# Kernel tuning notes

Hardware: AMD Instinct MI355X
Metric: run time of the kernel (lower is better)

The kernel has to match this reference:

```python
import jax, jax.numpy as jnp
from jax import lax
import numpy as np

B, S, E, HID = 16, 7, 64, 64
RES = (64, 64); D = RES[0] * RES[1]
XLOW, XHIGH = -0.5, 0.5
RLOW, RHIGH = float(np.sqrt(0.01)), float(np.sqrt(0.05))
PIXEL_MULT = 1.0; N_ITER = 3; TSOFT = 1.0 / float(np.sqrt(E))

def _build_grid():
    ranges = [np.linspace(XLOW, XHIGH, r) for r in RES]
    g = np.stack(np.meshgrid(*ranges, indexing='xy'), axis=-1)
    g = g.reshape(RES[0], RES[1], -1).reshape(1, -1, 2)
    return jnp.asarray(g, dtype=jnp.float32)

ABS_GRID = _build_grid()  # [1, D, 2]

def _ln(x, g, b):
    m = jnp.mean(x, -1, keepdims=True)
    v = jnp.mean(jnp.square(x - m), -1, keepdims=True)
    return (x - m) * lax.rsqrt(v + 1e-5) * g + b

def _forward(data, slot_noise, pos_rand, conv0_w, conv0_b, conv1_w, conv1_b, conv2_w, conv2_b,
             dataN_g, dataN_b, queryN_g, queryN_b, toK_w, toK_b, toV_w, toV_b, dense_w, dense_b,
             mlp1_w, mlp1_b, mlp2_w, mlp2_b, gru_wih, gru_whh, gru_bih, gru_bhh,
             alpha1_w, alpha1_b, alpha2_w, alpha2_b, final1_w, final1_b, final2_w, final2_b,
             slots_mu, slots_logsigma):
    dn = ('NCHW', 'OIHW', 'NCHW')
    def conv(x, w, b):
        return lax.conv_general_dilated(x, w, (1, 1), 'SAME', dimension_numbers=dn) + b[None, :, None, None]
    # CNN encoder: Conv-ReLU x3, 'same' padding, k=5
    x = jax.nn.relu(conv(data, conv0_w, conv0_b))
    x = jax.nn.relu(conv(x, conv1_w, conv1_b))
    x = jax.nn.relu(conv(x, conv2_w, conv2_b))
    enc = x.transpose(0, 2, 3, 1).reshape(B, D, HID)
    enc = _ln(enc, dataN_g, dataN_b)

    queries = slots_mu + jnp.exp(slots_logsigma) * slot_noise  # [B,S,E]
    # init_slots: faithful replication (source indexes the SLOT dim, and swaps rlow/rhigh)
    pos_scale = pos_rand.at[:, :2, :].add(-0.5)
    pos_scale = pos_scale.at[:, -1, :].set((RLOW - RHIGH) * pos_rand[:, -1, :] + RHIGH)

    encK = enc @ toK_w + toK_b  # [B,D,E]
    encV = enc @ toV_w + toV_b

    def init_mlp(y):
        y = _ln(y, queryN_g, queryN_b)
        return jax.nn.relu(y @ mlp1_w + mlp1_b) @ mlp2_w + mlp2_b

    def get_kv(ps):
        # per-slot relative grid: [B,S,D,2]
        rel = (ABS_GRID[:, None] - ps[:, :, None, :2]) / ps[:, :, -1][:, :, None, None]
        eg = PIXEL_MULT * (rel @ dense_w + dense_b)  # [B,S,D,E]
        return init_mlp(encK[:, None] + eg), init_mlp(encV[:, None] + eg)

    def att_wts(q, k):
        logits = jnp.einsum('bse,bsde->bsd', q, k) * TSOFT
        att = jax.nn.softmax(logits, axis=1)  # softmax over slots
        wts = att / jnp.sum(att, -1, keepdims=True) + 1e-8
        return att, wts

    def update_frames(wts):
        new_pos = jnp.einsum('bsd,de->bse', wts, ABS_GRID[0])  # [B,S,2]
        d2 = jnp.sum(jnp.square(ABS_GRID[:, None] - new_pos[:, :, None]), -1)  # [B,S,D]
        new_scale = jnp.sqrt(jnp.einsum('bsd,bsd->bs', wts, d2))
        return jnp.concatenate([new_pos, new_scale[..., None]], -1)

    def gru(xg, h):
        gi = xg @ gru_wih.T + gru_bih
        gh = h @ gru_whh.T + gru_bhh
        ir, iz, inn = jnp.split(gi, 3, -1)
        hr, hz, hn = jnp.split(gh, 3, -1)
        r = jax.nn.sigmoid(ir + hr)
        z = jax.nn.sigmoid(iz + hz)
        n = jnp.tanh(inn + r * hn)
        return (1.0 - z) * n + z * h

    for _ in range(N_ITER):
        keys, vals = get_kv(pos_scale)
        att, wts = att_wts(_ln(queries, queryN_g, queryN_b), keys)
        pos_scale = update_frames(wts)
        upd = jnp.einsum('bsd,bsde->bse', wts, vals)
        queries = gru(upd.reshape(-1, E), queries.reshape(-1, E)).reshape(B, S, E)

    keys, _ = get_kv(pos_scale)
    att, wts = att_wts(_ln(queries, queryN_g, queryN_b), keys)
    nps = update_frames(wts)
    alpha = jax.nn.sigmoid(jax.nn.relu(queries @ alpha1_w + alpha1_b) @ alpha2_w + alpha2_b)
    slot_feat = jax.nn.relu(queries @ final1_w + final1_b) @ final2_w + final2_b + nps
    return queries, att, slot_feat, alpha

def setup_inputs() -> dict:
    ks = jax.random.split(jax.random.key(0), 20)
    f32 = jnp.float32
    def rn(i, shape, s):
        return jax.random.normal(ks[i], shape, f32) * s
    inp = dict(
        data=jax.random.normal(ks[0], (B, 1, RES[0], RES[1]), f32),
        slot_noise=jax.random.normal(ks[1], (B, S, E), f32),
        pos_rand=jax.random.uniform(ks[2], (B, S, 3), dtype=f32),
        conv0_w=rn(3, (HID, 1, 5, 5), 0.2), conv0_b=jnp.zeros(HID, f32),
        conv1_w=rn(4, (HID, HID, 5, 5), 0.025), conv1_b=jnp.zeros(HID, f32),
        conv2_w=rn(5, (HID, HID, 5, 5), 0.025), conv2_b=jnp.zeros(HID, f32),
        dataN_g=jnp.ones(HID, f32), dataN_b=jnp.zeros(HID, f32),
        queryN_g=jnp.ones(E, f32), queryN_b=jnp.zeros(E, f32),
        toK_w=rn(6, (HID, E), 0.125), toK_b=jnp.zeros(E, f32),
        toV_w=rn(7, (HID, E), 0.125), toV_b=jnp.zeros(E, f32),
        dense_w=rn(8, (2, E), 0.7), dense_b=jnp.zeros(E, f32),
        mlp1_w=rn(9, (E, E), 0.125), mlp1_b=jnp.zeros(E, f32),
        mlp2_w=rn(10, (E, E), 0.125), mlp2_b=jnp.zeros(E, f32),
        gru_wih=rn(11, (3 * E, E), 0.125), gru_whh=rn(12, (3 * E, E), 0.125),
        gru_bih=jnp.zeros(3 * E, f32), gru_bhh=jnp.zeros(3 * E, f32),
        alpha1_w=rn(13, (E, 32), 0.125), alpha1_b=jnp.zeros(32, f32),
        alpha2_w=rn(14, (32, 1), 0.18), alpha2_b=jnp.zeros(1, f32),
        final1_w=rn(15, (E, HID), 0.125), final1_b=jnp.zeros(HID, f32),
        final2_w=rn(16, (HID, 3), 0.125), final2_b=jnp.zeros(3, f32),
        slots_mu=rn(17, (1, 1, E), 1.0),
        slots_logsigma=rn(18, (1, 1, E), 0.01),
    )
    return inp

def reference(data, slot_noise, pos_rand, conv0_w, conv0_b, conv1_w, conv1_b, conv2_w, conv2_b,
              dataN_g, dataN_b, queryN_g, queryN_b, toK_w, toK_b, toV_w, toV_b, dense_w, dense_b,
              mlp1_w, mlp1_b, mlp2_w, mlp2_b, gru_wih, gru_whh, gru_bih, gru_bhh,
              alpha1_w, alpha1_b, alpha2_w, alpha2_b, final1_w, final1_b, final2_w, final2_b,
              slots_mu, slots_logsigma):
    return _forward(data, slot_noise, pos_rand, conv0_w, conv0_b, conv1_w, conv1_b, conv2_w, conv2_b,
                    dataN_g, dataN_b, queryN_g, queryN_b, toK_w, toK_b, toV_w, toV_b, dense_w, dense_b,
                    mlp1_w, mlp1_b, mlp2_w, mlp2_b, gru_wih, gru_whh, gru_bih, gru_bhh,
                    alpha1_w, alpha1_b, alpha2_w, alpha2_b, final1_w, final1_b, final2_w, final2_b,
                    slots_mu, slots_logsigma)
```

## Files before the change

### kernel.cpp

```cpp
#include <hip/hip_runtime.h>
#include <cmath>


#define RLOW_F 0.1f
#define RHIGH_F 0.22360679774997896f
#define W0CONST 1.00004096f
#define SR2 704.3386243f

typedef __attribute__((ext_vector_type(8))) __bf16 bf16x8;
typedef __attribute__((ext_vector_type(4))) float f32x4;

__device__ __forceinline__ float wsum64(float v){
  #pragma unroll
  for (int off = 32; off > 0; off >>= 1) v += __shfl_xor(v, off, 64);
  return v;
}
__device__ __forceinline__ float rdlane(float v, int l){
  return __int_as_float(__builtin_amdgcn_readlane(__float_as_int(v), l));
}
__device__ __forceinline__ unsigned short bf16bits(float v){
  __bf16 h = (__bf16)v;
  return *reinterpret_cast<unsigned short*>(&h);
}

__device__ __forceinline__ void pp_core(int row, int e, float qv,
    float px, float py, float sc,
    const float* __restrict__ qg_, const float* __restrict__ qb_,
    const float* __restrict__ dw, const float* __restrict__ db,
    const float* __restrict__ mlp2w, const float* __restrict__ mlp2b,
    float* __restrict__ absc, float* __restrict__ w2qc){
  float m = wsum64(qv) * (1.f/64.f);
  float d = qv - m;
  float var = wsum64(d*d) * (1.f/64.f);
  float qlnv = d * (1.0f/sqrtf(var + 1e-5f)) * qg_[e] + qb_[e];
  float A  = dw[e]      / sc;
  float Bv = dw[64 + e] / sc;
  absc[row*192 + e]       = A;
  absc[row*192 + 64 + e]  = Bv;
  absc[row*192 + 128 + e] = db[e] - px*A - py*Bv;
  float acc = 0.f;
  const float* wrow = mlp2w + e*64;
  for (int j = 0; j < 64; j++) acc = fmaf(wrow[j], rdlane(qlnv, j), acc);
  w2qc[row*68 + e] = acc;
  float c2 = wsum64(mlp2b[e] * qlnv);
  if (e == 0) w2qc[row*68 + 64] = c2;
}

__global__ void k_packall(const float* __restrict__ mlp1_w, const float* __restrict__ toK_w,
                          const float* __restrict__ toV_w, const float* __restrict__ conv1_w,
                          const float* __restrict__ conv2_w,
                          unsigned short* __restrict__ w1pack, unsigned short* __restrict__ kpack,
                          unsigned short* __restrict__ vpack, unsigned short* __restrict__ wp1,
                          unsigned short* __restrict__ wp2,
                          const float* __restrict__ noise, const float* __restrict__ prand,
                          const float* __restrict__ mu, const float* __restrict__ logsig,
                          const float* __restrict__ qg_, const float* __restrict__ qb_,
                          const float* __restrict__ dw, const float* __restrict__ db,
                          const float* __restrict__ mlp2w, const float* __restrict__ mlp2b,
                          float* __restrict__ queries, float* __restrict__ ps,
                          float* __restrict__ absc, float* __restrict__ w2qc,
                          float* __restrict__ accF, float* __restrict__ upd){
  int bi = blockIdx.x; int t = threadIdx.x;
  if (bi < 48){
    const float* src = (bi < 16) ? mlp1_w : ((bi < 32) ? toK_w : toV_w);
    unsigned short* dst = (bi < 16) ? w1pack : ((bi < 32) ? kpack : vpack);
    int idx = (bi & 15)*256 + t;
    int jj = idx & 7;
    int lane = (idx >> 3) & 63;
    int frag = idx >> 9;
    int ks = frag >> 2, nt = frag & 3;
    int q = lane >> 4, cr = lane & 15;
    int k = ks*32 + q*8 + jj;
    int n = nt*16 + cr;
    dst[idx] = bf16bits(src[k*64 + n]);
  } else if (bi < 848){
    int rb = bi - 48;
    const float* src = (rb < 400) ? conv1_w : conv2_w;
    unsigned short* dst = (rb < 400) ? wp1 : wp2;
    int idx = (rb % 400)*256 + t;
    int j = idx & 7;
    int l = (idx >> 3) & 63;
    int frag = idx >> 9;
    int nt = frag & 3;
    int ks = (frag >> 2) % 10;
    int dy = frag / 40;
    int q = l >> 4, cr = l & 15;
    int k = ks*32 + q*8 + j;
    int kx = k >> 6, ch = k & 63;
    int n = nt*16 + cr;
    dst[idx] = bf16bits(src[((n*64 + ch)*5 + dy)*5 + kx]);
  } else {
    if (t >= 64) return;
    int row = bi - 848;
    int e = t;
    int s = row % 7;
    float qv = mu[e] + expf(logsig[e]) * noise[row*64 + e];
    queries[row*64 + e] = qv;
    upd[row*128 + e] = 0.f;
    upd[row*128 + 64 + e] = 0.f;
    if (e < 4) accF[row*4 + e] = 0.f;
    float pv = 0.f;
    if (e < 3){
      float pr = prand[row*3 + e];
      if (s < 2)       pv = pr - 0.5f;
      else if (s == 6) pv = (RLOW_F - RHIGH_F)*pr + RHIGH_F;
      else             pv = pr;
      ps[row*3 + e] = pv;
    }
    float px = rdlane(pv, 0), py = rdlane(pv, 1), sc = rdlane(pv, 2);
    pp_core(row, e, qv, px, py, sc, qg_, qb_, dw, db, mlp2w, mlp2b, absc, w2qc);
  }
}

__global__ __launch_bounds__(256) void k_conv0(const float* __restrict__ in,
                        const float* __restrict__ w, const float* __restrict__ bias,
                        unsigned short* __restrict__ out){
  int bi = blockIdx.x; int b = bi >> 6; int y = bi & 63;
  int t = threadIdx.x; int lane = t & 63; int xg = t >> 6;
  __shared__ float s_in[5*68];
  __shared__ float s_w[64*25];
  __shared__ float s_out[64*65];
  for (int i = t; i < 1600; i += 256) s_w[i] = w[i];
  for (int i = t; i < 340; i += 256){
    int r = i / 68, cx = i % 68;
    int yy = y + r - 2, gx = cx - 2;
    float v = 0.f;
// ... 141 lines not shown
  const bf16x8* vp = reinterpret_cast<const bf16x8*>(vpack);
  bf16x8 KB[8], VB[8];
  #pragma unroll
  for (int f = 0; f < 8; f++){ KB[f] = kp[f*64 + l]; VB[f] = vp[f*64 + l]; }

  const unsigned short* er = enc + (size_t)(b*4096 + d0 + cr)*64;
  bf16x8 a0 = *reinterpret_cast<const bf16x8*>(er + q*8);
  bf16x8 a1 = *reinterpret_cast<const bf16x8*>(er + 32 + q*8);

  f32x4 zero = {0.f,0.f,0.f,0.f};
  f32x4 aK[4], aV[4];
  #pragma unroll
  for (int nt = 0; nt < 4; nt++){
    aK[nt] = __builtin_amdgcn_mfma_f32_16x16x32_bf16(a0, KB[nt],     zero,   0, 0, 0);
    aK[nt] = __builtin_amdgcn_mfma_f32_16x16x32_bf16(a1, KB[4 + nt], aK[nt], 0, 0, 0);
    aV[nt] = __builtin_amdgcn_mfma_f32_16x16x32_bf16(a0, VB[nt],     zero,   0, 0, 0);
    aV[nt] = __builtin_amdgcn_mfma_f32_16x16x32_bf16(a1, VB[4 + nt], aV[nt], 0, 0, 0);
  }
  #pragma unroll
  for (int nt = 0; nt < 4; nt++){
    float bkv = bk[nt*16 + cr], bvv = bvp[nt*16 + cr];
    #pragma unroll
    for (int reg = 0; reg < 4; reg++){
      size_t base = ((size_t)b*4096 + d0 + q*4 + reg)*64 + nt*16 + cr;
      K[base] = bf16bits(aK[nt][reg] + bkv);
      V[base] = bf16bits(aV[nt][reg] + bvv);
    }
  }
}

__global__ __launch_bounds__(256) void k_attn(const unsigned short* __restrict__ encK,
     const unsigned short* __restrict__ encV,
     const unsigned short* __restrict__ w1pack, const float* __restrict__ mlp1b,
     const float* __restrict__ absc, const float* __restrict__ qg_,
     const float* __restrict__ qb_, const float* __restrict__ w2qc,
     float* __restrict__ attOut, float* __restrict__ accF,
     float* __restrict__ upd, int mode){
  int bi = blockIdx.x;
  int b = bi >> 6, tile = bi & 63;
  int t = threadIdx.x; int wv = t >> 6; int l = t & 63;
  int q = l >> 4, cr = l & 15;
  int m0 = tile*64 + wv*16;
  int drow = m0 + cr;

  __shared__ float s_log[7*64];
  __shared__ float s_absc[7*192];
  __shared__ float s_wq[7*68];
  __shared__ float s_upd[7*128];
  __shared__ unsigned short s_w1[4096];
  for (int i = t; i < 1344; i += 256) s_absc[i] = absc[b*7*192 + i];
  for (int i = t; i < 476;  i += 256) s_wq[i]   = w2qc[b*7*68 + i];
  if (mode == 0)
    for (int i = t; i < 896; i += 256) s_upd[i] = 0.f;
  {
    const uint4* g = reinterpret_cast<const uint4*>(w1pack);
    uint4* d = reinterpret_cast<uint4*>(s_w1);
    for (int i = t; i < 512; i += 256) d[i] = g[i];
  }

  const unsigned short* er = encK + (size_t)(b*4096 + drow)*64;
  float gx = -0.5f + (float)(drow & 63) * (1.f/63.f);
  float gy = -0.5f + (float)((drow >> 6) & 63) * (1.f/63.f);
  float xb[16], gq[16], bq[16];
  {
    bf16x8 ea = *reinterpret_cast<const bf16x8*>(er + q*8);
    bf16x8 eb = *reinterpret_cast<const bf16x8*>(er + 32 + q*8);
    #pragma unroll
    for (int i = 0; i < 8; i++){ xb[i] = (float)ea[i]; xb[8+i] = (float)eb[i]; }
  }
  bf16x8 vb0, vb1;
  if (mode == 0){
    const unsigned short* ev = encV + (size_t)(b*4096 + drow)*64;
    vb0 = *reinterpret_cast<const bf16x8*>(ev + q*8);
    vb1 = *reinterpret_cast<const bf16x8*>(ev + 32 + q*8);
  }
  #pragma unroll
  for (int h = 0; h < 2; h++){
    int fb = h ? (32 + q*8) : (q*8);
    const float4* g4 = reinterpret_cast<const float4*>(qg_ + fb);
    const float4* b4 = reinterpret_cast<const float4*>(qb_ + fb);
    #pragma unroll
    for (int p = 0; p < 2; p++){
      float4 gg = g4[p], bb = b4[p];
      int o = h*8 + p*4;
      gq[o+0]=gg.x; gq[o+1]=gg.y; gq[o+2]=gg.z; gq[o+3]=gg.w;
      bq[o+0]=bb.x; bq[o+1]=bb.y; bq[o+2]=bb.z; bq[o+3]=bb.w;
    }
  }
  float b1v[4];
  #pragma unroll
  for (int nt = 0; nt < 4; nt++) b1v[nt] = mlp1b[nt*16 + cr];
  __syncthreads();

  const bf16x8* wl = reinterpret_cast<const bf16x8*>(s_w1);
  f32x4 zero = {0.f, 0.f, 0.f, 0.f};

  for (int sp = 0; sp < 4; sp++){
    int s0 = sp*2;
    int np = (sp == 3) ? 1 : 2;
    int sB = (np == 2) ? s0 + 1 : s0;
    float x0[16], x1[16];
    float s1a = 0.f, s2a = 0.f, s1b = 0.f, s2b = 0.f;
    {
      const float* Ac = s_absc + s0*192;
      #pragma unroll
      for (int h = 0; h < 2; h++){
        int fb = h ? (32 + q*8) : (q*8);
        const float4* A4 = reinterpret_cast<const float4*>(Ac + fb);
        const float4* B4 = reinterpret_cast<const float4*>(Ac + 64 + fb);
        const float4* C4 = reinterpret_cast<const float4*>(Ac + 128 + fb);
        #pragma unroll
        for (int p = 0; p < 2; p++){
          float4 Av = A4[p], Bv = B4[p], Cv = C4[p];
          int o = h*8 + p*4;
          x0[o+0] = xb[o+0] + gx*Av.x + gy*Bv.x + Cv.x;
          x0[o+1] = xb[o+1] + gx*Av.y + gy*Bv.y + Cv.y;
          x0[o+2] = xb[o+2] + gx*Av.z + gy*Bv.z + Cv.z;
          x0[o+3] = xb[o+3] + gx*Av.w + gy*Bv.w + Cv.w;
        }
      }
      #pragma unroll
      for (int k = 0; k < 16; k++){ s1a += x0[k]; s2a = fmaf(x0[k], x0[k], s2a); }
    }
    {
      const float* Ac = s_absc + sB*192;
      #pragma unroll
      for (int h = 0; h < 2; h++){
        int fb = h ? (32 + q*8) : (q*8);
        const float4* A4 = reinterpret_cast<const float4*>(Ac + fb);
        const float4* B4 = reinterpret_cast<const float4*>(Ac + 64 + fb);
        const float4* C4 = reinterpret_cast<const float4*>(Ac + 128 + fb);
        #pragma unroll
        for (int p = 0; p < 2; p++){
          float4 Av = A4[p], Bv = B4[p], Cv = C4[p];
          int o = h*8 + p*4;
          x1[o+0] = xb[o+0] + gx*Av.x + gy*Bv.x + Cv.x;
          x1[o+1] = xb[o+1] + gx*Av.y + gy*Bv.y + Cv.y;
          x1[o+2] = xb[o+2] + gx*Av.z + gy*Bv.z + Cv.z;
          x1[o+3] = xb[o+3] + gx*Av.w + gy*Bv.w + Cv.w;
        }
      }
      #pragma unroll
      for (int k = 0; k < 16; k++){ s1b += x1[k]; s2b = fmaf(x1[k], x1[k], s2b); }
    }
    s1a += __shfl_xor(s1a, 16, 64); s2a += __shfl_xor(s2a, 16, 64);
    s1b += __shfl_xor(s1b, 16, 64); s2b += __shfl_xor(s2b, 16, 64);
    s1a += __shfl_xor(s1a, 32, 64); s2a += __shfl_xor(s2a, 32, 64);
    s1b += __shfl_xor(s1b, 32, 64); s2b += __shfl_xor(s2b, 32, 64);
    float mA = s1a*(1.f/64.f);
    float rA = 1.0f/sqrtf(s2a*(1.f/64.f) - mA*mA + 1e-5f);
    float mB = s1b*(1.f/64.f);
    float rB = 1.0f/sqrtf(s2b*(1.f/64.f) - mB*mB + 1e-5f);

    bf16x8 a00, a01, a10, a11;
    #pragma unroll
    for (int k = 0; k < 8; k++){
      a00[k] = (__bf16)((x0[k]    - mA)*rA*gq[k]   + bq[k]);
      a01[k] = (__bf16)((x0[8+k]  - mA)*rA*gq[8+k] + bq[8+k]);
      a10[k] = (__bf16)((x1[k]    - mB)*rB*gq[k]   + bq[k]);
      a11[k] = (__bf16)((x1[8+k]  - mB)*rB*gq[8+k] + bq[8+k]);
    }

    f32x4 acc0[4], acc1[4];
    #pragma unroll
    for (int nt = 0; nt < 4; nt++){
      bf16x8 w0 = wl[nt*64 + l];
      bf16x8 w1f = wl[(4 + nt)*64 + l];
      acc0[nt] = __builtin_amdgcn_mfma_f32_16x16x32_bf16(a00, w0,  zero,     0, 0, 0);
      acc0[nt] = __builtin_amdgcn_mfma_f32_16x16x32_bf16(a01, w1f, acc0[nt], 0, 0, 0);
      acc1[nt] = __builtin_amdgcn_mfma_f32_16x16x32_bf16(a10, w0,  zero,     0, 0, 0);
      acc1[nt] = __builtin_amdgcn_mfma_f32_16x16x32_bf16(a11, w1f, acc1[nt], 0, 0, 0);
    }

    float p0[4] = {0.f,0.f,0.f,0.f}, p1[4] = {0.f,0.f,0.f,0.f};
    #pragma unroll
    for (int nt = 0; nt < 4; nt++){
      float wq0 = s_wq[s0*68 + nt*16 + cr];
      float wq1 = s_wq[sB*68 + nt*16 + cr];
      #pragma unroll
      for (int reg = 0; reg < 4; reg++){
        p0[reg] = fmaf(fmaxf(acc0[nt][reg] + b1v[nt], 0.f), wq0, p0[reg]);
        p1[reg] = fmaf(fmaxf(acc1[nt][reg] + b1v[nt], 0.f), wq1, p1[reg]);
      }
    }
    #pragma unroll
    for (int off = 1; off < 16; off <<= 1){
      #pragma unroll
      for (int reg = 0; reg < 4; reg++){
        p0[reg] += __shfl_xor(p0[reg], off, 64);
        p1[reg] += __shfl_xor(p1[reg], off, 64);
      }
    }
    if (cr == 0){
      float c20 = s_wq[s0*68 + 64];
      float c21 = s_wq[sB*68 + 64];
      #pragma unroll
      for (int reg = 0; reg < 4; reg++){
        s_log[s0*64 + wv*16 + q*4 + reg] = (p0[reg] + c20) * 0.125f;
        if (np == 2) s_log[sB*64 + wv*16 + q*4 + reg] = (p1[reg] + c21) * 0.125f;
      }
    }
  }
  __syncthreads();

  if (t < 64){
    float lv[7];
    #pragma unroll
    for (int s = 0; s < 7; s++) lv[s] = s_log[s*64 + t];
    float mx = lv[0];
    #pragma unroll
    for (int s = 1; s < 7; s++) mx = fmaxf(mx, lv[s]);
    float sm = 0.f;
    #pragma unroll
    for (int s = 0; s < 7; s++){ lv[s] = expf(lv[s] - mx); sm += lv[s]; }
    float inv = 1.0f / sm;
    #pragma unroll
    for (int s = 0; s < 7; s++){
      float a = lv[s] * inv;
      s_log[s*64 + t] = a;
      if (mode == 1) attOut[(size_t)(b*7+s)*4096 + tile*64 + t] = a;
    }
  }
  __syncthreads();

  if (t < 224){
    int s = t >> 5, r = t & 31;
    float a1 = s_log[s*64 + r];
    float a2 = s_log[s*64 + r + 32];
    float gx1 = -0.5f + (float)r * (1.f/63.f);
    float gx2 = -0.5f + (float)(r + 32) * (1.f/63.f);
    float gyc = -0.5f + (float)tile * (1.f/63.f);
    float gy2c = gyc*gyc;
    float w0 = a1 + a2;
    float w1 = a1*gx1 + a2*gx2;
    float w2 = w0*gyc;
    float w3 = a1*(gx1*gx1 + gy2c) + a2*(gx2*gx2 + gy2c);
    #pragma unroll
    for (int m = 1; m < 32; m <<= 1){
      w0 += __shfl_xor(w0, m, 64);
      w1 += __shfl_xor(w1, m, 64);
      w2 += __shfl_xor(w2, m, 64);
      w3 += __shfl_xor(w3, m, 64);
    }
    if (r == 0){
      atomicAdd(&accF[(b*7+s)*4 + 0], w0);
      atomicAdd(&accF[(b*7+s)*4 + 1], w1);
      atomicAdd(&accF[(b*7+s)*4 + 2], w2);
      atomicAdd(&accF[(b*7+s)*4 + 3], w3);
    }
  }

  if (mode == 0){
    float xbv[16];
    #pragma unroll
    for (int i = 0; i < 8; i++){ xbv[i] = (float)vb0[i]; xbv[8+i] = (float)vb1[i]; }
    for (int sp = 0; sp < 4; sp++){
      int s0 = sp*2;
      int np = (sp == 3) ? 1 : 2;
      int sB = (np == 2) ? s0 + 1 : s0;
      float x0[16], x1[16];
      float s1a = 0.f, s2a = 0.f, s1b = 0.f, s2b = 0.f;
      {
        const float* Ac = s_absc + s0*192;
        #pragma unroll
        for (int h = 0; h < 2; h++){
          int fb = h ? (32 + q*8) : (q*8);
          const float4* A4 = reinterpret_cast<const float4*>(Ac + fb);
          const float4* B4 = reinterpret_cast<const float4*>(Ac + 64 + fb);
          const float4* C4 = reinterpret_cast<const float4*>(Ac + 128 + fb);
          #pragma unroll
          for (int p = 0; p < 2; p++){
            float4 Av = A4[p], Bv = B4[p], Cv = C4[p];
            int o = h*8 + p*4;
            x0[o+0] = xbv[o+0] + gx*Av.x + gy*Bv.x + Cv.x;
            x0[o+1] = xbv[o+1] + gx*Av.y + gy*Bv.y + Cv.y;
            x0[o+2] = xbv[o+2] + gx*Av.z + gy*Bv.z + Cv.z;
            x0[o+3] = xbv[o+3] + gx*Av.w + gy*Bv.w + Cv.w;
          }
        }
        #pragma unroll
        for (int k = 0; k < 16; k++){ s1a += x0[k]; s2a = fmaf(x0[k], x0[k], s2a); }
      }
      {
        const float* Ac = s_absc + sB*192;
        #pragma unroll
        for (int h = 0; h < 2; h++){
          int fb = h ? (32 + q*8) : (q*8);
          const float4* A4 = reinterpret_cast<const float4*>(Ac + fb);
          const float4* B4 = reinterpret_cast<const float4*>(Ac + 64 + fb);
          const float4* C4 = reinterpret_cast<const float4*>(Ac + 128 + fb);
          #pragma unroll
          for (int p = 0; p < 2; p++){
            float4 Av = A4[p], Bv = B4[p], Cv = C4[p];
            int o = h*8 + p*4;
            x1[o+0] = xbv[o+0] + gx*Av.x + gy*Bv.x + Cv.x;
            x1[o+1] = xbv[o+1] + gx*Av.y + gy*Bv.y + Cv.y;
            x1[o+2] = xbv[o+2] + gx*Av.z + gy*Bv.z + Cv.z;
            x1[o+3] = xbv[o+3] + gx*Av.w + gy*Bv.w + Cv.w;
          }
        }
        #pragma unroll
        for (int k = 0; k < 16; k++){ s1b += x1[k]; s2b = fmaf(x1[k], x1[k], s2b); }
      }
      s1a += __shfl_xor(s1a, 16, 64); s2a += __shfl_xor(s2a, 16, 64);
      s1b += __shfl_xor(s1b, 16, 64); s2b += __shfl_xor(s2b, 16, 64);
      s1a += __shfl_xor(s1a, 32, 64); s2a += __shfl_xor(s2a, 32, 64);
      s1b += __shfl_xor(s1b, 32, 64); s2b += __shfl_xor(s2b, 32, 64);
      float mA = s1a*(1.f/64.f);
      float rA = 1.0f/sqrtf(s2a*(1.f/64.f) - mA*mA + 1e-5f);
      float mB = s1b*(1.f/64.f);
      float rB = 1.0f/sqrtf(s2b*(1.f/64.f) - mB*mB + 1e-5f);

      bf16x8 a00, a01, a10, a11;
      #pragma unroll
      for (int k = 0; k < 8; k++){
        a00[k] = (__bf16)((x0[k]    - mA)*rA*gq[k]   + bq[k]);
        a01[k] = (__bf16)((x0[8+k]  - mA)*rA*gq[8+k] + bq[8+k]);
        a10[k] = (__bf16)((x1[k]    - mB)*rB*gq[k]   + bq[k]);
        a11[k] = (__bf16)((x1[8+k]  - mB)*rB*gq[8+k] + bq[8+k]);
      }

      f32x4 acc0[4], acc1[4];
      #pragma unroll
      for (int nt = 0; nt < 4; nt++){
        bf16x8 w0 = wl[nt*64 + l];
        bf16x8 w1f = wl[(4 + nt)*64 + l];
        acc0[nt] = __builtin_amdgcn_mfma_f32_16x16x32_bf16(a00, w0,  zero,     0, 0, 0);
        acc0[nt] = __builtin_amdgcn_mfma_f32_16x16x32_bf16(a01, w1f, acc0[nt], 0, 0, 0);
        acc1[nt] = __builtin_amdgcn_mfma_f32_16x16x32_bf16(a10, w0,  zero,     0, 0, 0);
        acc1[nt] = __builtin_amdgcn_mfma_f32_16x16x32_bf16(a11, w1f, acc1[nt], 0, 0, 0);
      }

      float wr0[4], wr1[4];
      #pragma unroll
      for (int reg = 0; reg < 4; reg++){
        wr0[reg] = s_log[s0*64 + wv*16 + q*4 + reg];
        wr1[reg] = s_log[sB*64 + wv*16 + q*4 + reg];
      }
      float pa0[4], pa1[4], pu0[4], pu1[4];
      #pragma unroll
      for (int nt = 0; nt < 4; nt++){
        pa0[nt] = 0.f; pa1[nt] = 0.f; pu0[nt] = 0.f; pu1[nt] = 0.f;
        #pragma unroll
        for (int reg = 0; reg < 4; reg++){
          float v0 = fmaxf(acc0[nt][reg] + b1v[nt], 0.f);
          float v1 = fmaxf(acc1[nt][reg] + b1v[nt], 0.f);
          pa0[nt] = fmaf(wr0[reg], v0, pa0[nt]); pu0[nt] += v0;
          pa1[nt] = fmaf(wr1[reg], v1, pa1[nt]); pu1[nt] += v1;
        }
      }
      #pragma unroll
      for (int nt = 0; nt < 4; nt++){
        pa0[nt] += __shfl_xor(pa0[nt], 16, 64); pa0[nt] += __shfl_xor(pa0[nt], 32, 64);
        pu0[nt] += __shfl_xor(pu0[nt], 16, 64); pu0[nt] += __shfl_xor(pu0[nt], 32, 64);
        pa1[nt] += __shfl_xor(pa1[nt], 16, 64); pa1[nt] += __shfl_xor(pa1[nt], 32, 64);
        pu1[nt] += __shfl_xor(pu1[nt], 16, 64); pu1[nt] += __shfl_xor(pu1[nt], 32, 64);
      }
      if (q == 0){
        #pragma unroll
        for (int nt = 0; nt < 4; nt++){
          atomicAdd(&s_upd[s0*128 + nt*16 + cr], pa0[nt]);
          atomicAdd(&s_upd[s0*128 + 64 + nt*16 + cr], pu0[nt]);
          if (np == 2){
            atomicAdd(&s_upd[sB*128 + nt*16 + cr], pa1[nt]);
            atomicAdd(&s_upd[sB*128 + 64 + nt*16 + cr], pu1[nt]);
          }
        }
      }
    }
    __syncthreads();
    for (int i = t; i < 896; i += 256)
      atomicAdd(&upd[b*896 + i], s_upd[i]);
  }
}

__global__ void k_gru(float* __restrict__ upd, float* __restrict__ queries,
                      const float* __restrict__ wih, const float* __restrict__ whh,
                      const float* __restrict__ bih, const float* __restrict__ bhh,
                      const float* __restrict__ mlp2w, const float* __restrict__ mlp2b,
                      float* __restrict__ accF, float* __restrict__ ps,
                      const float* __restrict__ qg_, const float* __restrict__ qb_,
                      const float* __restrict__ dw, const float* __restrict__ db,
                      float* __restrict__ absc, float* __restrict__ w2qc){
  int row = blockIdx.x; int t = threadIdx.x;
  __shared__ float us[64], hs[64], xs[64], gis[192], ghs[192];
  __shared__ float s_ps3[3];
  if (t < 64){
    float isa0 = 1.0f/accF[row*4];
    us[t] = upd[row*128 + t]*isa0 + 1e-8f*upd[row*128 + 64 + t];
    hs[t] = queries[row*64 + t];
  }
  if (t == 64){
    float sa = accF[row*4+0];
    float ax = accF[row*4+1], ay = accF[row*4+2], ar2 = accF[row*4+3];
    float isa = 1.0f/sa;
    float Wx = ax*isa, Wy = ay*isa;
    float Wg = ar2*isa + 1e-8f*SR2;
    float s2 = Wg - (Wx*Wx + Wy*Wy)*(2.f - W0CONST);
    s_ps3[0] = Wx; s_ps3[1] = Wy; s_ps3[2] = sqrtf(fmaxf(s2, 0.f));
  }
  __syncthreads();
  if (t < 64){
    float a = W0CONST * mlp2b[t];
    for (int i = 0; i < 64; i++) a = fmaf(us[i], mlp2w[i*64 + t], a);
    xs[t] = a;
  }
  __syncthreads();
  float gi = bih[t], gh = bhh[t];
  for (int e = 0; e < 64; e++){
    gi = fmaf(wih[t*64 + e], xs[e], gi);
    gh = fmaf(whh[t*64 + e], hs[e], gh);
  }
  gis[t] = gi; ghs[t] = gh;
  __syncthreads();
  if (t < 64){
    float r = 1.0f/(1.0f + expf(-(gis[t]      + ghs[t])));
    float z = 1.0f/(1.0f + expf(-(gis[64+t]   + ghs[64+t])));
    float n = tanhf(gis[128+t] + r*ghs[128+t]);
    float newq = (1.0f - z)*n + z*hs[t];
    queries[row*64 + t] = newq;
    upd[row*128 + t] = 0.f;
    upd[row*128 + 64 + t] = 0.f;
    if (t < 4) accF[row*4 + t] = 0.f;
    if (t < 3) ps[row*3 + t] = s_ps3[t];
    pp_core(row, t, newq, s_ps3[0], s_ps3[1], s_ps3[2],
            qg_, qb_, dw, db, mlp2w, mlp2b, absc, w2qc);
  }
}

__global__ void k_final(const float* __restrict__ queries, const float* __restrict__ accF,
                        const float* __restrict__ a1w, const float* __restrict__ a1b,
                        const float* __restrict__ a2w, const float* __restrict__ a2b,
                        const float* __restrict__ f1w, const float* __restrict__ f1b,
                        const float* __restrict__ f2w, const float* __restrict__ f2b,
                        float* __restrict__ out){
  int bs = blockIdx.x; int e = threadIdx.x;
  __shared__ float qs[64], hf[64], ha[32];
  float q = queries[bs*64 + e];
  qs[e] = q;
  out[bs*64 + e] = q;
  __syncthreads();
  float accf = f1b[e];
  for (int i = 0; i < 64; i++) accf = fmaf(qs[i], f1w[i*64 + e], accf);
  hf[e] = fmaxf(accf, 0.f);
  if (e < 32){
    float acca = a1b[e];
    for (int i = 0; i < 64; i++) acca = fmaf(qs[i], a1w[i*32 + e], acca);
    ha[e] = fmaxf(acca, 0.f);
  }
  __syncthreads();
  if (e < 3){
    float sf = f2b[e];
    for (int o = 0; o < 64; o++) sf = fmaf(hf[o], f2w[o*3 + e], sf);
    float sa = accF[bs*4+0], ax = accF[bs*4+1], ay = accF[bs*4+2], ar2 = accF[bs*4+3];
    float isa = 1.0f/sa;
    float Wx = ax*isa, Wy = ay*isa;
    float Wg = ar2*isa + 1e-8f*SR2;
    float s2 = Wg - (Wx*Wx + Wy*Wy)*(2.f - W0CONST);
    float nv = (e == 0) ? Wx : ((e == 1) ? Wy : sqrtf(fmaxf(s2, 0.f)));
    out[465920 + bs*3 + e] = sf + nv;
  }
  if (e == 32){
    float al = a2b[0];
    for (int o = 0; o < 32; o++) al = fmaf(ha[o], a2w[o], al);
    out[466256 + bs] = 1.0f/(1.0f + expf(-al));
  }
}

extern "C" void kernel_launch(void* const* d_in, const int* in_sizes, int n_in,
                              void* d_out, int out_size, void* d_ws, size_t ws_size,
                              hipStream_t stream){
  const float* data        = (const float*)d_in[0];
  const float* slot_noise  = (const float*)d_in[1];
  const float* pos_rand    = (const float*)d_in[2];
  const float* conv0_w     = (const float*)d_in[3];
  const float* conv0_b     = (const float*)d_in[4];
  const float* conv1_w     = (const float*)d_in[5];
  const float* conv1_b     = (const float*)d_in[6];
  const float* conv2_w     = (const float*)d_in[7];
  const float* conv2_b     = (const float*)d_in[8];
  const float* dataN_g     = (const float*)d_in[9];
  const float* dataN_b     = (const float*)d_in[10];
  const float* queryN_g    = (const float*)d_in[11];
  const float* queryN_b    = (const float*)d_in[12];
  const float* toK_w       = (const float*)d_in[13];
  const float* toK_b       = (const float*)d_in[14];
  const float* toV_w       = (const float*)d_in[15];
  const float* toV_b       = (const float*)d_in[16];
  const float* dense_w     = (const float*)d_in[17];
  const float* dense_b     = (const float*)d_in[18];
  const float* mlp1_w      = (const float*)d_in[19];
  const float* mlp1_b      = (const float*)d_in[20];
  const float* mlp2_w      = (const float*)d_in[21];
  const float* mlp2_b      = (const float*)d_in[22];
  const float* gru_wih     = (const float*)d_in[23];
  const float* gru_whh     = (const float*)d_in[24];
  const float* gru_bih     = (const float*)d_in[25];
  const float* gru_bhh     = (const float*)d_in[26];
  const float* alpha1_w    = (const float*)d_in[27];
  const float* alpha1_b    = (const float*)d_in[28];
  const float* alpha2_w    = (const float*)d_in[29];
  const float* alpha2_b    = (const float*)d_in[30];
  const float* final1_w    = (const float*)d_in[31];
  const float* final1_b    = (const float*)d_in[32];
  const float* final2_w    = (const float*)d_in[33];
  const float* final2_b    = (const float*)d_in[34];
  const float* slots_mu    = (const float*)d_in[35];
  const float* slots_lsig  = (const float*)d_in[36];

  float* ws   = (float*)d_ws;
  float* bufA = ws;
  float* bufB = bufA + 4194304;
  float* bufC = bufB + 4194304;
  float* queries = bufC + 4194304;
  float* ps   = queries + 7168;
  float* absc = ps + 512;
  float* accF = absc + 21504;
  float* upd  = accF + 512;
  float* w2qc = upd + 14336;
  unsigned short* w1pack = (unsigned short*)(w2qc + 7616);
  unsigned short* kpack  = w1pack + 4096;
  unsigned short* vpack  = kpack + 4096;
  unsigned short* wp1    = vpack + 4096;
  unsigned short* wp2    = wp1 + 102400;

  unsigned short* c0_bf = (unsigned short*)bufA;
  unsigned short* c1_bf = (unsigned short*)bufC;
  unsigned short* enc   = (unsigned short*)bufB;
  unsigned short* encK  = (unsigned short*)bufA;
  unsigned short* encV  = (unsigned short*)bufC;

  float* outq   = (float*)d_out;
  float* outatt = outq + 7168;

  k_packall<<<960, 256, 0, stream>>>(mlp1_w, toK_w, toV_w, conv1_w, conv2_w,
                                     w1pack, kpack, vpack, wp1, wp2,
                                     slot_noise, pos_rand, slots_mu, slots_lsig,
                                     queryN_g, queryN_b, dense_w, dense_b, mlp2_w, mlp2_b,
                                     queries, ps, absc, w2qc, accF, upd);
  k_conv0<<<1024, 256, 0, stream>>>(data, conv0_w, conv0_b, c0_bf);
  k_convm<<<512, 256, 0, stream>>>(c0_bf, wp1, conv1_b, nullptr, nullptr, c1_bf, 0);
  k_convm<<<512, 256, 0, stream>>>(c1_bf, wp2, conv2_b, dataN_g, dataN_b, enc, 1);
  k_projm<<<1024, 256, 0, stream>>>(enc, kpack, toK_b, vpack, toV_b, encK, encV);

  for (int p = 0; p < 4; p++){
    k_attn<<<1024, 256, 0, stream>>>(encK, encV, w1pack, mlp1_b, absc,
                                     queryN_g, queryN_b, w2qc, outatt, accF, upd,
                                     (p < 3) ? 0 : 1);
    if (p < 3){
      k_gru<<<112, 192, 0, stream>>>(upd, queries, gru_wih, gru_whh, gru_bih, gru_bhh,
                                     mlp2_w, mlp2_b, accF, ps, queryN_g, queryN_b,
                                     dense_w, dense_b, absc, w2qc);
    }
  }
  k_final<<<112, 64, 0, stream>>>(queries, accF,
                                  alpha1_w, alpha1_b, alpha2_w, alpha2_b,
                                  final1_w, final1_b, final2_w, final2_b, outq);
}
```

Baseline: 486.6 us.

## Fuse GRU update and final heads into attention kernel via last-block counter

Removes the separate k_gru and k_final launches. Each k_attn block increments a per-batch atomic counter after its atomic accumulation, and the last of the 64 tiles for a batch then runs the GRU update (or the final heads in the last pass) for all 7 slots of that batch. This cuts four kernel launches and the gaps between them. In exchange, the tail work runs in a single block per batch with serialized loops, the kernel adds shared memory that may lower occupancy, and it relies on threadfence plus atomic reads for correctness.

```diff
diff --git a/kernel.cpp b/kernel.cpp
--- a/kernel.cpp
+++ b/kernel.cpp
@@ -21,6 +21,9 @@
 __device__ __forceinline__ unsigned short bf16bits(float v){
   __bf16 h = (__bf16)v;
   return *reinterpret_cast<unsigned short*>(&h);
+}
+__device__ __forceinline__ float aread(float* p){
+  return atomicAdd(p, 0.f);
 }
 
 __device__ __forceinline__ void pp_core(int row, int e, float qv,
@@ -59,7 +62,8 @@
                           const float* __restrict__ mlp2w, const float* __restrict__ mlp2b,
                           float* __restrict__ queries, float* __restrict__ ps,
                           float* __restrict__ absc, float* __restrict__ w2qc,
-                          float* __restrict__ accF, float* __restrict__ upd){
+                          float* __restrict__ accF, float* __restrict__ upd,
+                          unsigned int* __restrict__ cnt){
   int bi = blockIdx.x; int t = threadIdx.x;
   if (bi < 48){
     const float* src = (bi < 16) ? mlp1_w : ((bi < 32) ? toK_w : toV_w);
@@ -90,8 +94,9 @@
     int n = nt*16 + cr;
     dst[idx] = bf16bits(src[((n*64 + ch)*5 + dy)*5 + kx]);
   } else {
+    int row = bi - 848;
+    if (bi == 848 && t >= 64 && t < 80) cnt[t - 64] = 0u;
     if (t >= 64) return;
-    int row = bi - 848;
     int e = t;
     int s = row % 7;
     float qv = mu[e] + expf(logsig[e]) * noise[row*64 + e];
@@ -299,10 +304,20 @@
 __global__ __launch_bounds__(256) void k_attn(const unsigned short* __restrict__ encK,
      const unsigned short* __restrict__ encV,
      const unsigned short* __restrict__ w1pack, const float* __restrict__ mlp1b,
-     const float* __restrict__ absc, const float* __restrict__ qg_,
-     const float* __restrict__ qb_, const float* __restrict__ w2qc,
+     float* __restrict__ absc, const float* __restrict__ qg_,
+     const float* __restrict__ qb_, float* __restrict__ w2qc,
      float* __restrict__ attOut, float* __restrict__ accF,
-     float* __restrict__ upd, int mode){
+     float* __restrict__ upd, int mode, unsigned int* __restrict__ cnt,
+     float* __restrict__ queries, float* __restrict__ ps,
+     const float* __restrict__ wih, const float* __restrict__ whh,
+     const float* __restrict__ bih, const float* __restrict__ bhh,
+     const float* __restrict__ mlp2w, const float* __restrict__ mlp2b,
+     const float* __restrict__ dw, const float* __restrict__ db,
+     const float* __restrict__ a1w, const float* __restrict__ a1b,
+     const float* __restrict__ a2w, const float* __restrict__ a2b,
+     const float* __restrict__ f1w, const float* __restrict__ f1b,
+     const float* __restrict__ f2w, const float* __restrict__ f2b,
+     float* __restrict__ outq){
   int bi = blockIdx.x;
   int b = bi >> 6, tile = bi & 63;
   int t = threadIdx.x; int wv = t >> 6; int l = t & 63;
@@ -315,6 +330,11 @@
   __shared__ float s_wq[7*68];
   __shared__ float s_upd[7*128];
   __shared__ unsigned short s_w1[4096];
+  __shared__ float G_us[7][64], G_hs[7][64], G_xs[7][64];
+  __shared__ float G_gi[7][192], G_gh[7][192];
+  __shared__ float G_af[28], G_p3[7][3];
+  __shared__ unsigned s_last;
+
   for (int i = t; i < 1344; i += 256) s_absc[i] = absc[b*7*192 + i];
   for (int i = t; i < 476;  i += 256) s_wq[i]   = w2qc[b*7*68 + i];
   if (mode == 0)
@@ -377,9 +397,9 @@
         const float4* B4 = reinterpret_cast<const float4*>(Ac + 64 + fb);
         const float4* C4 = reinterpret_cast<const float4*>(Ac + 128 + fb);
         #pragma unroll
-        for (int p = 0; p < 2; p++){
-          float4 Av = A4[p], Bv = B4[p], Cv = C4[p];
-          int o = h*8 + p*4;
+        for (int pp = 0; pp < 2; pp++){
+          float4 Av = A4[pp], Bv = B4[pp], Cv = C4[pp];
+          int o = h*8 + pp*4;
           x0[o+0] = xb[o+0] + gx*Av.x + gy*Bv.x + Cv.x;
           x0[o+1] = xb[o+1] + gx*Av.y + gy*Bv.y + Cv.y;
           x0[o+2] = xb[o+2] + gx*Av.z + gy*Bv.z + Cv.z;
@@ -398,9 +418,9 @@
         const float4* B4 = reinterpret_cast<const float4*>(Ac + 64 + fb);
         const float4* C4 = reinterpret_cast<const float4*>(Ac + 128 + fb);
         #pragma unroll
-        for (int p = 0; p < 2; p++){
-          float4 Av = A4[p], Bv = B4[p], Cv = C4[p];
-          int o = h*8 + p*4;
+        for (int pp = 0; pp < 2; pp++){
+          float4 Av = A4[pp], Bv = B4[pp], Cv = C4[pp];
+          int o = h*8 + pp*4;
           x1[o+0] = xb[o+0] + gx*Av.x + gy*Bv.x + Cv.x;
           x1[o+1] = xb[o+1] + gx*Av.y + gy*Bv.y + Cv.y;
           x1[o+2] = xb[o+2] + gx*Av.z + gy*Bv.z + Cv.z;
@@ -536,9 +556,9 @@
           const float4* B4 = reinterpret_cast<const float4*>(Ac + 64 + fb);
           const float4* C4 = reinterpret_cast<const float4*>(Ac + 128 + fb);
           #pragma unroll
-          for (int p = 0; p < 2; p++){
-            float4 Av = A4[p], Bv = B4[p], Cv = C4[p];
-            int o = h*8 + p*4;
+          for (int pp = 0; pp < 2; pp++){
+            float4 Av = A4[pp], Bv = B4[pp], Cv = C4[pp];
+            int o = h*8 + pp*4;
             x0[o+0] = xbv[o+0] + gx*Av.x + gy*Bv.x + Cv.x;
             x0[o+1] = xbv[o+1] + gx*Av.y + gy*Bv.y + Cv.y;
             x0[o+2] = xbv[o+2] + gx*Av.z + gy*Bv.z + Cv.z;
@@ -557,9 +577,9 @@
           const float4* B4 = reinterpret_cast<const float4*>(Ac + 64 + fb);
           const float4* C4 = reinterpret_cast<const float4*>(Ac + 128 + fb);
           #pragma unroll
-          for (int p = 0; p < 2; p++){
-            float4 Av = A4[p], Bv = B4[p], Cv = C4[p];
-            int o = h*8 + p*4;
+          for (int pp = 0; pp < 2; pp++){
+            float4 Av = A4[pp], Bv = B4[pp], Cv = C4[pp];
+            int o = h*8 + pp*4;
             x1[o+0] = xbv[o+0] + gx*Av.x + gy*Bv.x + Cv.x;
             x1[o+1] = xbv[o+1] + gx*Av.y + gy*Bv.y + Cv.y;
             x1[o+2] = xbv[o+2] + gx*Av.z + gy*Bv.z + Cv.z;
@@ -639,98 +659,110 @@
     for (int i = t; i < 896; i += 256)
       atomicAdd(&upd[b*896 + i], s_upd[i]);
   }
-}
-
-__global__ void k_gru(float* __restrict__ upd, float* __restrict__ queries,
-                      const float* __restrict__ wih, const float* __restrict__ whh,
-                      const float* __restrict__ bih, const float* __restrict__ bhh,
-                      const float* __restrict__ mlp2w, const float* __restrict__ mlp2b,
-                      float* __restrict__ accF, float* __restrict__ ps,
-                      const float* __restrict__ qg_, const float* __restrict__ qb_,
-                      const float* __restrict__ dw, const float* __restrict__ db,
-                      float* __restrict__ absc, float* __restrict__ w2qc){
-  int row = blockIdx.x; int t = threadIdx.x;
-  __shared__ float us[64], hs[64], xs[64], gis[192], ghs[192];
-  __shared__ float s_ps3[3];
-  if (t < 64){
-    float isa0 = 1.0f/accF[row*4];
-    us[t] = upd[row*128 + t]*isa0 + 1e-8f*upd[row*128 + 64 + t];
-    hs[t] = queries[row*64 + t];
-  }
-  if (t == 64){
-    float sa = accF[row*4+0];
-    float ax = accF[row*4+1], ay = accF[row*4+2], ar2 = accF[row*4+3];
-    float isa = 1.0f/sa;
-    float Wx = ax*isa, Wy = ay*isa;
-    float Wg = ar2*isa + 1e-8f*SR2;
-    float s2 = Wg - (Wx*Wx + Wy*Wy)*(2.f - W0CONST);
-    s_ps3[0] = Wx; s_ps3[1] = Wy; s_ps3[2] = sqrtf(fmaxf(s2, 0.f));
-  }
+
+  __threadfence();
   __syncthreads();
-  if (t < 64){
-    float a = W0CONST * mlp2b[t];
-    for (int i = 0; i < 64; i++) a = fmaf(us[i], mlp2w[i*64 + t], a);
-    xs[t] = a;
-  }
+  if (t == 0) s_last = (atomicAdd(&cnt[b], 1u) == 63u) ? 1u : 0u;
   __syncthreads();
-  float gi = bih[t], gh = bhh[t];
-  for (int e = 0; e < 64; e++){
-    gi = fmaf(wih[t*64 + e], xs[e], gi);
-    gh = fmaf(whh[t*64 + e], hs[e], gh);
-  }
-  gis[t] = gi; ghs[t] = gh;
-  __syncthreads();
-  if (t < 64){
-    float r = 1.0f/(1.0f + expf(-(gis[t]      + ghs[t])));
-    float z = 1.0f/(1.0f + expf(-(gis[64+t]   + ghs[64+t])));
-    float n = tanhf(gis[128+t] + r*ghs[128+t]);
-    float newq = (1.0f - z)*n + z*hs[t];
-    queries[row*64 + t] = newq;
-    upd[row*128 + t] = 0.f;
-    upd[row*128 + 64 + t] = 0.f;
-    if (t < 4) accF[row*4 + t] = 0.f;
-    if (t < 3) ps[row*3 + t] = s_ps3[t];
-    pp_core(row, t, newq, s_ps3[0], s_ps3[1], s_ps3[2],
-            qg_, qb_, dw, db, mlp2w, mlp2b, absc, w2qc);
-  }
-}
-
-__global__ void k_final(const float* __restrict__ queries, const float* __restrict__ accF,
-                        const float* __restrict__ a1w, const float* __restrict__ a1b,
-                        const float* __restrict__ a2w, const float* __restrict__ a2b,
-                        const float* __restrict__ f1w, const float* __restrict__ f1b,
-                        const float* __restrict__ f2w, const float* __restrict__ f2b,
-                        float* __restrict__ out){
-  int bs = blockIdx.x; int e = threadIdx.x;
-  __shared__ float qs[64], hf[64], ha[32];
-  float q = queries[bs*64 + e];
-  qs[e] = q;
-  out[bs*64 + e] = q;
-  __syncthreads();
-  float accf = f1b[e];
-  for (int i = 0; i < 64; i++) accf = fmaf(qs[i], f1w[i*64 + e], accf);
-  hf[e] = fmaxf(accf, 0.f);
-  if (e < 32){
-    float acca = a1b[e];
-    for (int i = 0; i < 64; i++) acca = fmaf(qs[i], a1w[i*32 + e], acca);
-    ha[e] = fmaxf(acca, 0.f);
-  }
-  __syncthreads();
-  if (e < 3){
-    float sf = f2b[e];
-    for (int o = 0; o < 64; o++) sf = fmaf(hf[o], f2w[o*3 + e], sf);
-    float sa = accF[bs*4+0], ax = accF[bs*4+1], ay = accF[bs*4+2], ar2 = accF[bs*4+3];
-    float isa = 1.0f/sa;
-    float Wx = ax*isa, Wy = ay*isa;
-    float Wg = ar2*isa + 1e-8f*SR2;
-    float s2 = Wg - (Wx*Wx + Wy*Wy)*(2.f - W0CONST);
-    float nv = (e == 0) ? Wx : ((e == 1) ? Wy : sqrtf(fmaxf(s2, 0.f)));
-    out[465920 + bs*3 + e] = sf + nv;
-  }
-  if (e == 32){
-    float al = a2b[0];
-    for (int o = 0; o < 32; o++) al = fmaf(ha[o], a2w[o], al);
-    out[466256 + bs] = 1.0f/(1.0f + expf(-al));
+  if (!s_last) return;
+  if (t == 0) atomicExch(&cnt[b], 0u);
+
+  if (mode == 0){
+    if (t < 28) G_af[t] = aread(&accF[b*28 + t]);
+    __syncthreads();
+    for (int i = t; i < 448; i += 256){
+      int r = i >> 6, e = i & 63; int row = b*7 + r;
+      float isa0 = 1.0f / G_af[r*4];
+      float u1 = aread(&upd[row*128 + e]);
+      float u2 = aread(&upd[row*128 + 64 + e]);
+      G_us[r][e] = u1*isa0 + 1e-8f*u2;
+      G_hs[r][e] = queries[row*64 + e];
+    }
+    if (t < 7){
+      float sa = G_af[t*4], ax = G_af[t*4+1], ay = G_af[t*4+2], ar2 = G_af[t*4+3];
+      float isa = 1.0f/sa;
+      float Wx = ax*isa, Wy = ay*isa;
+      float Wg = ar2*isa + 1e-8f*SR2;
+      float s2 = Wg - (Wx*Wx + Wy*Wy)*(2.f - W0CONST);
+      G_p3[t][0] = Wx; G_p3[t][1] = Wy; G_p3[t][2] = sqrtf(fmaxf(s2, 0.f));
+    }
+    __syncthreads();
+    for (int i = t; i < 448; i += 256){
+      int r = i >> 6, e = i & 63;
+      float a = W0CONST * mlp2b[e];
+      for (int j = 0; j < 64; j++) a = fmaf(G_us[r][j], mlp2w[j*64 + e], a);
+      G_xs[r][e] = a;
+    }
+    __syncthreads();
+    for (int i = t; i < 1344; i += 256){
+      int r = i / 192, tt = i % 192;
+      float gi = bih[tt], gh = bhh[tt];
+      for (int e = 0; e < 64; e++){
+        gi = fmaf(wih[tt*64 + e], G_xs[r][e], gi);
+        gh = fmaf(whh[tt*64 + e], G_hs[r][e], gh);
+      }
+      G_gi[r][tt] = gi; G_gh[r][tt] = gh;
+    }
+    __syncthreads();
+    for (int i = t; i < 448; i += 256){
+      int r = i >> 6, e = i & 63; int row = b*7 + r;
+      float rr = 1.0f/(1.0f + expf(-(G_gi[r][e]      + G_gh[r][e])));
+      float z  = 1.0f/(1.0f + expf(-(G_gi[r][64+e]   + G_gh[r][64+e])));
+      float n  = tanhf(G_gi[r][128+e] + rr*G_gh[r][128+e]);
+      float newq = (1.0f - z)*n + z*G_hs[r][e];
+      G_us[r][e] = newq;
+      queries[row*64 + e] = newq;
+      upd[row*128 + e] = 0.f;
+      upd[row*128 + 64 + e] = 0.f;
+    }
+    if (t < 28) accF[b*28 + t] = 0.f;
+    if (t < 21) ps[b*21 + t] = G_p3[t/3][t%3];
+    __syncthreads();
+    for (int rr = wv; rr < 7; rr += 4){
+      int row = b*7 + rr;
+      pp_core(row, l, G_us[rr][l], G_p3[rr][0], G_p3[rr][1], G_p3[rr][2],
+              qg_, qb_, dw, db, mlp2w, mlp2b, absc, w2qc);
+    }
+  } else {
+    if (t < 28) G_af[t] = aread(&accF[b*28 + t]);
+    for (int i = t; i < 448; i += 256){
+      int r = i >> 6, e = i & 63; int row = b*7 + r;
+      float qv = queries[row*64 + e];
+      G_us[r][e] = qv;
+      outq[row*64 + e] = qv;
+    }
+    __syncthreads();
+    for (int i = t; i < 448; i += 256){
+      int r = i >> 6, e = i & 63;
+      float a = f1b[e];
+      for (int j = 0; j < 64; j++) a = fmaf(G_us[r][j], f1w[j*64 + e], a);
+      G_hs[r][e] = fmaxf(a, 0.f);
+    }
+    for (int i = t; i < 224; i += 256){
+      int r = i >> 5, e = i & 31;
+      float a = a1b[e];
+      for (int j = 0; j < 64; j++) a = fmaf(G_us[r][j], a1w[j*32 + e], a);
+      G_xs[0][r*32 + e] = fmaxf(a, 0.f);
+    }
+    __syncthreads();
+    if (t < 21){
+      int r = t / 3, e = t % 3; int row = b*7 + r;
+      float sf = f2b[e];
+      for (int o = 0; o < 64; o++) sf = fmaf(G_hs[r][o], f2w[o*3 + e], sf);
+      float sa = G_af[r*4], ax = G_af[r*4+1], ay = G_af[r*4+2], ar2 = G_af[r*4+3];
+      float isa = 1.0f/sa;
+      float Wx = ax*isa, Wy = ay*isa;
+      float Wg = ar2*isa + 1e-8f*SR2;
+      float s2 = Wg - (Wx*Wx + Wy*Wy)*(2.f - W0CONST);
+      float nv = (e == 0) ? Wx : ((e == 1) ? Wy : sqrtf(fmaxf(s2, 0.f)));
+      outq[465920 + row*3 + e] = sf + nv;
+    }
+    if (t >= 32 && t < 39){
+      int r = t - 32; int row = b*7 + r;
+      float al = a2b[0];
+      for (int o = 0; o < 32; o++) al = fmaf(G_xs[0][r*32 + o], a2w[o], al);
+      outq[466256 + row] = 1.0f/(1.0f + expf(-al));
+    }
   }
 }
 
@@ -790,6 +822,7 @@
   unsigned short* vpack  = kpack + 4096;
   unsigned short* wp1    = vpack + 4096;
   unsigned short* wp2    = wp1 + 102400;
+  unsigned int*   cnt    = (unsigned int*)(wp2 + 102400);
 
   unsigned short* c0_bf = (unsigned short*)bufA;
   unsigned short* c1_bf = (unsigned short*)bufC;
@@ -804,7 +837,7 @@
                                      w1pack, kpack, vpack, wp1, wp2,
                                      slot_noise, pos_rand, slots_mu, slots_lsig,
                                      queryN_g, queryN_b, dense_w, dense_b, mlp2_w, mlp2_b,
-                                     queries, ps, absc, w2qc, accF, upd);
+                                     queries, ps, absc, w2qc, accF, upd, cnt);
   k_conv0<<<1024, 256, 0, stream>>>(data, conv0_w, conv0_b, c0_bf);
   k_convm<<<512, 256, 0, stream>>>(c0_bf, wp1, conv1_b, nullptr, nullptr, c1_bf, 0);
   k_convm<<<512, 256, 0, stream>>>(c1_bf, wp2, conv2_b, dataN_g, dataN_b, enc, 1);
@@ -813,14 +846,10 @@
   for (int p = 0; p < 4; p++){
     k_attn<<<1024, 256, 0, stream>>>(encK, encV, w1pack, mlp1_b, absc,
                                      queryN_g, queryN_b, w2qc, outatt, accF, upd,
-                                     (p < 3) ? 0 : 1);
-    if (p < 3){
-      k_gru<<<112, 192, 0, stream>>>(upd, queries, gru_wih, gru_whh, gru_bih, gru_bhh,
-                                     mlp2_w, mlp2_b, accF, ps, queryN_g, queryN_b,
-                                     dense_w, dense_b, absc, w2qc);
-    }
-  }
-  k_final<<<112, 64, 0, stream>>>(queries, accF,
-                                  alpha1_w, alpha1_b, alpha2_w, alpha2_b,
-                                  final1_w, final1_b, final2_w, final2_b, outq);
-}
+                                     (p < 3) ? 0 : 1, cnt, queries, ps,
+                                     gru_wih, gru_whh, gru_bih, gru_bhh,
+                                     mlp2_w, mlp2_b, dense_w, dense_b,
+                                     alpha1_w, alpha1_b, alpha2_w, alpha2_b,
+                                     final1_w, final1_b, final2_w, final2_b, outq);
+  }
+}
```

After: 793.2 us. 1.63x slower.

## Split attention work across waves by slot pairs and halve rows per block

Applied to the files above, without the earlier changes.

Each k_attn block now covers 32 pixel rows instead of 64, and the launch grid doubles to 2048 blocks. The four waves are split into two row halves times two slot-pair groups, so each wave runs two slot-pair iterations instead of four. This shortens the serial per-wave loop and raises the number of blocks in flight. In exchange, each block reloads the shared weights and constants for half as many rows, so per-block setup and global reduction work roughly doubles.

```diff
diff --git a/kernel.cpp b/kernel.cpp
--- a/kernel.cpp
+++ b/kernel.cpp
@@ -304,13 +304,14 @@
      float* __restrict__ attOut, float* __restrict__ accF,
      float* __restrict__ upd, int mode){
   int bi = blockIdx.x;
-  int b = bi >> 6, tile = bi & 63;
+  int b = bi >> 7, tile = bi & 127;
   int t = threadIdx.x; int wv = t >> 6; int l = t & 63;
   int q = l >> 4, cr = l & 15;
-  int m0 = tile*64 + wv*16;
+  int rowHalf = wv & 1, spg = wv >> 1;
+  int m0 = tile*32 + rowHalf*16;
   int drow = m0 + cr;
 
-  __shared__ float s_log[7*64];
+  __shared__ float s_log[7*32];
   __shared__ float s_absc[7*192];
   __shared__ float s_wq[7*68];
   __shared__ float s_upd[7*128];
@@ -362,7 +363,8 @@
   const bf16x8* wl = reinterpret_cast<const bf16x8*>(s_w1);
   f32x4 zero = {0.f, 0.f, 0.f, 0.f};
 
-  for (int sp = 0; sp < 4; sp++){
+  for (int spi = 0; spi < 2; spi++){
+    int sp = spg*2 + spi;
     int s0 = sp*2;
     int np = (sp == 3) ? 1 : 2;
     int sB = (np == 2) ? s0 + 1 : s0;
@@ -377,9 +379,9 @@
         const float4* B4 = reinterpret_cast<const float4*>(Ac + 64 + fb);
         const float4* C4 = reinterpret_cast<const float4*>(Ac + 128 + fb);
         #pragma unroll
-        for (int p = 0; p < 2; p++){
-          float4 Av = A4[p], Bv = B4[p], Cv = C4[p];
-          int o = h*8 + p*4;
+        for (int pp = 0; pp < 2; pp++){
+          float4 Av = A4[pp], Bv = B4[pp], Cv = C4[pp];
+          int o = h*8 + pp*4;
           x0[o+0] = xb[o+0] + gx*Av.x + gy*Bv.x + Cv.x;
           x0[o+1] = xb[o+1] + gx*Av.y + gy*Bv.y + Cv.y;
           x0[o+2] = xb[o+2] + gx*Av.z + gy*Bv.z + Cv.z;
@@ -398,9 +400,9 @@
         const float4* B4 = reinterpret_cast<const float4*>(Ac + 64 + fb);
         const float4* C4 = reinterpret_cast<const float4*>(Ac + 128 + fb);
         #pragma unroll
-        for (int p = 0; p < 2; p++){
-          float4 Av = A4[p], Bv = B4[p], Cv = C4[p];
-          int o = h*8 + p*4;
+        for (int pp = 0; pp < 2; pp++){
+          float4 Av = A4[pp], Bv = B4[pp], Cv = C4[pp];
+          int o = h*8 + pp*4;
           x1[o+0] = xb[o+0] + gx*Av.x + gy*Bv.x + Cv.x;
           x1[o+1] = xb[o+1] + gx*Av.y + gy*Bv.y + Cv.y;
           x1[o+2] = xb[o+2] + gx*Av.z + gy*Bv.z + Cv.z;
@@ -463,17 +465,17 @@
       float c21 = s_wq[sB*68 + 64];
       #pragma unroll
       for (int reg = 0; reg < 4; reg++){
-        s_log[s0*64 + wv*16 + q*4 + reg] = (p0[reg] + c20) * 0.125f;
-        if (np == 2) s_log[sB*64 + wv*16 + q*4 + reg] = (p1[reg] + c21) * 0.125f;
-      }
-    }
-  }
-  __syncthreads();
-
-  if (t < 64){
+        s_log[s0*32 + rowHalf*16 + q*4 + reg] = (p0[reg] + c20) * 0.125f;
+        if (np == 2) s_log[sB*32 + rowHalf*16 + q*4 + reg] = (p1[reg] + c21) * 0.125f;
+      }
+    }
+  }
+  __syncthreads();
+
+  if (t < 32){
     float lv[7];
     #pragma unroll
-    for (int s = 0; s < 7; s++) lv[s] = s_log[s*64 + t];
+    for (int s = 0; s < 7; s++) lv[s] = s_log[s*32 + t];
     float mx = lv[0];
     #pragma unroll
     for (int s = 1; s < 7; s++) mx = fmaxf(mx, lv[s]);
@@ -484,24 +486,22 @@
     #pragma unroll
     for (int s = 0; s < 7; s++){
       float a = lv[s] * inv;
-      s_log[s*64 + t] = a;
-      if (mode == 1) attOut[(size_t)(b*7+s)*4096 + tile*64 + t] = a;
+      s_log[s*32 + t] = a;
+      if (mode == 1) attOut[(size_t)(b*7+s)*4096 + tile*32 + t] = a;
     }
   }
   __syncthreads();
 
   if (t < 224){
     int s = t >> 5, r = t & 31;
-    float a1 = s_log[s*64 + r];
-    float a2 = s_log[s*64 + r + 32];
-    float gx1 = -0.5f + (float)r * (1.f/63.f);
-    float gx2 = -0.5f + (float)(r + 32) * (1.f/63.f);
-    float gyc = -0.5f + (float)tile * (1.f/63.f);
-    float gy2c = gyc*gyc;
-    float w0 = a1 + a2;
-    float w1 = a1*gx1 + a2*gx2;
-    float w2 = w0*gyc;
-    float w3 = a1*(gx1*gx1 + gy2c) + a2*(gx2*gx2 + gy2c);
+    float a1 = s_log[s*32 + r];
+    int dcol = tile*32 + r;
+    float gx1 = -0.5f + (float)(dcol & 63) * (1.f/63.f);
+    float gyc = -0.5f + (float)(dcol >> 6) * (1.f/63.f);
+    float w0 = a1;
+    float w1 = a1*gx1;
+    float w2 = a1*gyc;
+    float w3 = a1*(gx1*gx1 + gyc*gyc);
     #pragma unroll
     for (int m = 1; m < 32; m <<= 1){
       w0 += __shfl_xor(w0, m, 64);
@@ -521,7 +521,8 @@
     float xbv[16];
     #pragma unroll
     for (int i = 0; i < 8; i++){ xbv[i] = (float)vb0[i]; xbv[8+i] = (float)vb1[i]; }
-    for (int sp = 0; sp < 4; sp++){
+    for (int spi = 0; spi < 2; spi++){
+      int sp = spg*2 + spi;
       int s0 = sp*2;
       int np = (sp == 3) ? 1 : 2;
       int sB = (np == 2) ? s0 + 1 : s0;
@@ -536,9 +537,9 @@
           const float4* B4 = reinterpret_cast<const float4*>(Ac + 64 + fb);
           const float4* C4 = reinterpret_cast<const float4*>(Ac + 128 + fb);
           #pragma unroll
-          for (int p = 0; p < 2; p++){
-            float4 Av = A4[p], Bv = B4[p], Cv = C4[p];
-            int o = h*8 + p*4;
+          for (int pp = 0; pp < 2; pp++){
+            float4 Av = A4[pp], Bv = B4[pp], Cv = C4[pp];
+            int o = h*8 + pp*4;
             x0[o+0] = xbv[o+0] + gx*Av.x + gy*Bv.x + Cv.x;
             x0[o+1] = xbv[o+1] + gx*Av.y + gy*Bv.y + Cv.y;
             x0[o+2] = xbv[o+2] + gx*Av.z + gy*Bv.z + Cv.z;
@@ -557,9 +558,9 @@
           const float4* B4 = reinterpret_cast<const float4*>(Ac + 64 + fb);
           const float4* C4 = reinterpret_cast<const float4*>(Ac + 128 + fb);
           #pragma unroll
-          for (int p = 0; p < 2; p++){
-            float4 Av = A4[p], Bv = B4[p], Cv = C4[p];
-            int o = h*8 + p*4;
+          for (int pp = 0; pp < 2; pp++){
+            float4 Av = A4[pp], Bv = B4[pp], Cv = C4[pp];
+            int o = h*8 + pp*4;
             x1[o+0] = xbv[o+0] + gx*Av.x + gy*Bv.x + Cv.x;
             x1[o+1] = xbv[o+1] + gx*Av.y + gy*Bv.y + Cv.y;
             x1[o+2] = xbv[o+2] + gx*Av.z + gy*Bv.z + Cv.z;
@@ -601,8 +602,8 @@
       float wr0[4], wr1[4];
       #pragma unroll
       for (int reg = 0; reg < 4; reg++){
-        wr0[reg] = s_log[s0*64 + wv*16 + q*4 + reg];
-        wr1[reg] = s_log[sB*64 + wv*16 + q*4 + reg];
+        wr0[reg] = s_log[s0*32 + rowHalf*16 + q*4 + reg];
+        wr1[reg] = s_log[sB*32 + rowHalf*16 + q*4 + reg];
       }
       float pa0[4], pa1[4], pu0[4], pu1[4];
       #pragma unroll
@@ -811,7 +812,7 @@
   k_projm<<<1024, 256, 0, stream>>>(enc, kpack, toK_b, vpack, toV_b, encK, encV);
 
   for (int p = 0; p < 4; p++){
-    k_attn<<<1024, 256, 0, stream>>>(encK, encV, w1pack, mlp1_b, absc,
+    k_attn<<<2048, 256, 0, stream>>>(encK, encV, w1pack, mlp1_b, absc,
                                      queryN_g, queryN_b, w2qc, outatt, accF, upd,
                                      (p < 3) ? 0 : 1);
     if (p < 3){
```

After: 681.2 us. 1.4x slower.
